# Performance work log

Measured on AMD Instinct MI355X. Metric: run time of the kernel, lower is better.

The kernel has to match this reference:

```python
import jax, jax.numpy as jnp
import numpy as np

B, T, N, DIN, H, E, K, HM, CH, HOR, DOUT = 64, 12, 307, 1, 64, 10, 2, 16, 14, 12, 1
EPS = 1e-12


def setup_inputs() -> dict:
    key = jax.random.key(0)
    ks = jax.random.split(key, 16)
    rn = lambda k, s, sc=0.1: jax.random.normal(k, s, dtype=jnp.float32) * sc
    return {
        "hyper_source": jax.random.normal(ks[0], (B, CH, T, N), dtype=jnp.float32),
        "source": jax.random.normal(ks[1], (B, T, N, DIN), dtype=jnp.float32),
        "adj": jax.random.uniform(ks[2], (N, N), dtype=jnp.float32),
        "node_embeddings": rn(ks[3], (N, E), 1.0),
        "main_weights_pool": rn(ks[4], (E, H, DIN)),
        "hyper_W": rn(ks[5], (CH, H)),
        "hyper_b": jnp.zeros((H,), jnp.float32),
        "mask_W1": rn(ks[6], (H, HM)),
        "mask_W2": rn(ks[7], (HM, E)),
        "gate_Wpool": rn(ks[8], (E, K, 2 * DIN + H, 2 * H)),
        "gate_bpool": rn(ks[9], (E, 2 * H)),
        "upd_Wpool": rn(ks[10], (E, K, 2 * DIN + H, H)),
        "upd_bpool": rn(ks[11], (E, H)),
        "ln_gamma": jnp.ones((H,), jnp.float32),
        "ln_beta": jnp.zeros((H,), jnp.float32),
        "end_W": rn(ks[12], (HOR * DOUT, H)),
        "end_b": jnp.zeros((HOR * DOUT,), jnp.float32),
    }


def _forward(hyper_source, source, adj, node_embeddings, main_weights_pool,
             hyper_W, hyper_b, mask_W1, mask_W2, gate_Wpool, gate_bpool,
             upd_Wpool, upd_bpool, ln_gamma, ln_beta, end_W, end_b):
    # HyperNet: chunked long-history signal -> per-node per-step hidden h [B,N,T,H]
    h = jnp.tanh(jnp.einsum('bctn,ch->bnth', hyper_source, hyper_W) + hyper_b)
    # adaptive input channel: einsum('bnld,ndi->blni') with per-node weights
    weights_h = jnp.einsum('nd,dhi->nhi', node_embeddings, main_weights_pool)  # [N,H,DIN]
    x_adapt = jnp.einsum('bnlh,nhi->blni', h, weights_h)                       # [B,T,N,DIN]
    x = jnp.concatenate([x_adapt, source], axis=-1)                            # [B,T,N,2*DIN]
    # static Chebyshev supports (cheb_k=2): identity + mix(normalized adj, adaptive graph)
    adj_n = adj / jnp.clip(adj.sum(-1, keepdims=True), 1e-6)
    adapt = jax.nn.softmax(jax.nn.relu(node_embeddings @ node_embeddings.T), axis=1)
    A = 0.5 * (adj_n + adapt)
    supports = jnp.stack([jnp.eye(N, dtype=x.dtype), A])                       # [K,N,N]
    # per-node graph-conv weights generated from node embeddings
    gate_W = jnp.einsum('nd,dkio->nkio', node_embeddings, gate_Wpool)
    gate_b = node_embeddings @ gate_bpool
    upd_W = jnp.einsum('nd,dkio->nkio', node_embeddings, upd_Wpool)
    upd_b = node_embeddings @ upd_bpool

    def gconv(sup_b, xin, Wn, bn):
        xg = jnp.einsum('bknm,bmi->bnki', sup_b, xin)
        return jnp.einsum('bnki,nkio->bno', xg, Wn) + bn

    def step(state, inp):
        xt, ht = inp  # [B,N,2*DIN], [B,N,H]
        # dynamic graph sparsification mask from hypernet state
        logits = jnp.einsum('bne,me->bnm', (ht @ mask_W1) @ mask_W2, node_embeddings)
        mask = jax.nn.sigmoid(logits)                # [B,N,N]
        sup_b = supports[None] * mask[:, None]       # [B,K,N,N]
        xs = jnp.concatenate([xt, state], axis=-1)
        zr = jax.nn.sigmoid(gconv(sup_b, xs, gate_W, gate_b))
        z, r = jnp.split(zr, 2, axis=-1)
        cand = jnp.concatenate([xt, z * state], axis=-1)
        hc = jnp.tanh(gconv(sup_b, cand, upd_W, upd_b))
        return r * state + (1.0 - r) * hc, None

    init = jnp.zeros((x.shape[0], N, H), x.dtype)
    state, _ = jax.lax.scan(step, init,
                            (jnp.swapaxes(x, 0, 1), jnp.transpose(h, (2, 0, 1, 3))))
    # layernorm(eps=1e-12); dropout is identity at eval
    mu = state.mean(-1, keepdims=True)
    var = ((state - mu) ** 2).mean(-1, keepdims=True)
    xn = (state - mu) / jnp.sqrt(var + EPS) * ln_gamma + ln_beta
    # end_conv: Conv2d(1, HOR*DOUT, kernel=(1,H)) == per-node linear H -> HOR*DOUT
    out = jnp.einsum('bnh,oh->bon', xn, end_W) + end_b[None, :, None]
    out = out.reshape(-1, HOR, DOUT, N).transpose(0, 1, 3, 2)  # [B,HOR,N,DOUT]
    return out


def reference(hyper_source, source, adj, node_embeddings, main_weights_pool,
              hyper_W, hyper_b, mask_W1, mask_W2, gate_Wpool, gate_bpool,
              upd_Wpool, upd_bpool, ln_gamma, ln_beta, end_W, end_b):
    return _forward(hyper_source, source, adj, node_embeddings, main_weights_pool,
                    hyper_W, hyper_b, mask_W1, mask_W2, gate_Wpool, gate_bpool,
                    upd_Wpool, upd_bpool, ln_gamma, ln_beta, end_W, end_b)
```

## Files before the change

### kernel.cpp

```cpp
#include <hip/hip_runtime.h>
#include <hip/hip_bf16.h>

#define N_ 307
#define B_ 64
#define T_ 12
#define H_ 64
#define E_ 10
#define CH_ 14
#define HM_ 16
#define I2_ 66
#define GO_ 128
#define UO_ 64
#define QG_ (2 * I2_ * GO_)
#define QU_ (2 * I2_ * UO_)

__device__ __forceinline__ float wsum(float v) {
    #pragma unroll
    for (int off = 32; off; off >>= 1) v += __shfl_xor(v, off);
    return v;
}
__device__ __forceinline__ float wmax(float v) {
    #pragma unroll
    for (int off = 32; off; off >>= 1) v = fmaxf(v, __shfl_xor(v, off));
    return v;
}
__device__ __forceinline__ float sigm(float x) { return 1.f / (1.f + __expf(-x)); }
__device__ __forceinline__ float ftanh(float x) { return 1.f - 2.f / (__expf(2.f * x) + 1.f); }

__global__ void A_kernel(const float* __restrict__ adj, const float* __restrict__ nemb,
                         float* __restrict__ A) {
    const int n = blockIdx.x;
    const int lane = threadIdx.x;
    float en[E_];
    #pragma unroll
    for (int d = 0; d < E_; ++d) en[d] = nemb[n * E_ + d];
    float asum = 0.f;
    for (int m = lane; m < N_; m += 64) asum += adj[n * N_ + m];
    asum = fmaxf(wsum(asum), 1e-6f);
    float g[5]; bool valid[5];
    float mx = -1e30f;
    #pragma unroll
    for (int it = 0; it < 5; ++it) {
        int m = lane + it * 64;
        valid[it] = (m < N_);
        float dt = 0.f;
        if (valid[it]) {
            #pragma unroll
            for (int e = 0; e < E_; ++e) dt += en[e] * nemb[m * E_ + e];
            dt = fmaxf(dt, 0.f);
            mx = fmaxf(mx, dt);
        }
        g[it] = dt;
    }
    mx = wmax(mx);
    float se = 0.f;
    #pragma unroll
    for (int it = 0; it < 5; ++it)
        if (valid[it]) { g[it] = __expf(g[it] - mx); se += g[it]; }
    se = wsum(se);
    float inv = 1.f / se;
    #pragma unroll
    for (int it = 0; it < 5; ++it) {
        int m = lane + it * 64;
        if (valid[it]) A[n * N_ + m] = 0.5f * (adj[n * N_ + m] / asum + g[it] * inv);
    }
}

__device__ __forceinline__ float embdot(const float* __restrict__ nemb, int n,
                                        const float* __restrict__ pool, int Q, int q) {
    float a = 0.f;
    #pragma unroll
    for (int d = 0; d < E_; ++d) a += nemb[n * E_ + d] * pool[d * Q + q];
    return a;
}

__global__ __launch_bounds__(256) void gen_kernel(
    const float* __restrict__ nemb,
    const float* __restrict__ gWp, const float* __restrict__ gbp,
    const float* __restrict__ uWp, const float* __restrict__ ubp,
    const float* __restrict__ mwp,
    const float* __restrict__ W1, const float* __restrict__ W2,
    float* __restrict__ gW, float* __restrict__ gb,
    float* __restrict__ uW, float* __restrict__ ub,
    float* __restrict__ wh, float* __restrict__ W12) {
    const int e0 = N_ * QG_;
    const int e1 = e0 + N_ * GO_;
    const int e2 = e1 + N_ * QU_;
    const int e3 = e2 + N_ * UO_;
    const int e4 = e3 + N_ * H_;
    const int e5 = e4 + H_ * E_;
    int idx = blockIdx.x * 256 + threadIdx.x;
    if (idx < e0) {
        int n = idx / QG_, q = idx % QG_;
        gW[idx] = embdot(nemb, n, gWp, QG_, q);
    } else if (idx < e1) {
        int i = idx - e0; int n = i / GO_, q = i % GO_;
        gb[i] = embdot(nemb, n, gbp, GO_, q);
    } else if (idx < e2) {
        int i = idx - e1; int n = i / QU_, q = i % QU_;
        uW[i] = embdot(nemb, n, uWp, QU_, q);
    } else if (idx < e3) {
        int i = idx - e2; int n = i / UO_, q = i % UO_;
        ub[i] = embdot(nemb, n, ubp, UO_, q);
    } else if (idx < e4) {
        int i = idx - e3; int n = i / H_, q = i % H_;
        wh[i] = embdot(nemb, n, mwp, H_, q);
    } else if (idx < e5) {
        int i = idx - e4; int j = i / E_, e = i % E_;
        float a = 0.f;
        #pragma unroll
        for (int q = 0; q < HM_; ++q) a += W1[j * HM_ + q] * W2[q * E_ + e];
        W12[i] = a;
    }
}

__global__ __launch_bounds__(256) void hyper_kernel(
    const float* __restrict__ hs, const float* __restrict__ src,
    const float* __restrict__ hyper_W, const float* __restrict__ hyper_b,
    const float* __restrict__ wh, const float* __restrict__ W12,
    float* __restrict__ x, float* __restrict__ emb) {
    const int wid = blockIdx.x * 4 + (threadIdx.x >> 6);
    const int lane = threadIdx.x & 63;
    const int t = wid / (B_ * N_);
    const int rem = wid % (B_ * N_);
    const int b = rem / N_;
    const int n = rem % N_;
    float acc = hyper_b[lane];
    #pragma unroll
    for (int c = 0; c < CH_; ++c)
        acc += hs[((b * CH_ + c) * T_ + t) * N_ + n] * hyper_W[c * H_ + lane];
    float h = ftanh(acc);
    float x0 = wsum(h * wh[n * H_ + lane]);
    float my_e = 0.f;
    #pragma unroll
    for (int e = 0; e < E_; ++e) {
        float ve = wsum(h * W12[lane * E_ + e]);
        if (lane == e) my_e = ve;
    }
    if (lane < E_) emb[wid * E_ + lane] = my_e;
    if (lane == 0) {
        x[wid * 2] = x0;
        x[wid * 2 + 1] = src[(b * T_ + t) * N_ + n];
    }
}

__global__ __launch_bounds__(256) void maskx_kernel(
    const float* __restrict__ A, const float* __restrict__ emb,
    const float* __restrict__ nemb, const float* __restrict__ x,
    float* __restrict__ dmask, float* __restrict__ aggx) {
    const int wid = blockIdx.x * 4 + (threadIdx.x >> 6);
    const int lane = threadIdx.x & 63;
    const int rem = wid % (B_ * N_);
    const int n = rem % N_;
    float et[E_];
    #pragma unroll
    for (int d = 0; d < E_; ++d) et[d] = emb[wid * E_ + d];
    float a0 = 0.f, a1 = 0.f;
    const int xbase = wid - n;
    for (int m = lane; m < N_; m += 64) {
        float dt = 0.f;
        #pragma unroll
        for (int d = 0; d < E_; ++d) dt += et[d] * nemb[m * E_ + d];
        float sg = sigm(dt);
        if (m == n) dmask[wid] = sg;
        float w = A[n * N_ + m] * sg;
        a0 += w * x[(xbase + m) * 2];
        a1 += w * x[(xbase + m) * 2 + 1];
    }
    a0 = wsum(a0);
    a1 = wsum(a1);
    if (lane == 0) { aggx[wid * 2] = a0; aggx[wid * 2 + 1] = a1; }
}

__global__ __launch_bounds__(256) void aggS_kernel(
    const float* __restrict__ A, const float* __restrict__ emb,
    const float* __restrict__ nemb, const float* __restrict__ Sin,
    float* __restrict__ aggS, int t) {
    __shared__ float emb_s[32][E_];
    __shared__ float ne_s[32][E_];
    __shared__ float w_s[32][33];
    __shared__ float s_s[32][64];
    const int n0 = blockIdx.x * 32;
    const int b = blockIdx.y;
    const int tid = threadIdx.x;
    for (int idx = tid; idx < 32 * E_; idx += 256) {
        int nl = idx / E_, d = idx % E_;
        int n = n0 + nl;
        emb_s[nl][d] = (n < N_) ? emb[((t * B_ + b) * N_ + n) * E_ + d] : 0.f;
    }
    const int ng = tid >> 4, ig = tid & 15;
    const int nl0 = ng * 2, i0 = ig * 4;
    float acc[2][4] = {};
    for (int m0 = 0; m0 < N_; m0 += 32) {
        __syncthreads();
        for (int idx = tid; idx < 32 * E_; idx += 256) {
            int ml = idx / E_, d = idx % E_;
            int m = m0 + ml;
            ne_s[ml][d] = (m < N_) ? nemb[m * E_ + d] : 0.f;
        }
        for (int idx = tid; idx < 32 * 64; idx += 256) {
            int ml = idx >> 6, i = idx & 63;
            int m = m0 + ml;
            s_s[ml][i] = (m < N_) ? Sin[(b * N_ + m) * 64 + i] : 0.f;
        }
        __syncthreads();
        for (int idx = tid; idx < 32 * 32; idx += 256) {
            int nl = idx >> 5, ml = idx & 31;
            int n = n0 + nl, m = m0 + ml;
            float w = 0.f;
            if (n < N_ && m < N_) {
                float dt = 0.f;
                #pragma unroll
                for (int e = 0; e < E_; ++e) dt += emb_s[nl][e] * ne_s[ml][e];
                w = A[n * N_ + m] * sigm(dt);
            }
            w_s[nl][ml] = w;
        }
        __syncthreads();
        #pragma unroll 8
        for (int ml = 0; ml < 32; ++ml) {
            float w0 = w_s[nl0][ml], w1 = w_s[nl0 + 1][ml];
            float4 sv = *(const float4*)&s_s[ml][i0];
            acc[0][0] += w0 * sv.x; acc[0][1] += w0 * sv.y;
            acc[0][2] += w0 * sv.z; acc[0][3] += w0 * sv.w;
            acc[1][0] += w1 * sv.x; acc[1][1] += w1 * sv.y;
            acc[1][2] += w1 * sv.z; acc[1][3] += w1 * sv.w;
        }
    }
    #pragma unroll
    for (int r = 0; r < 2; ++r) {
        int n = n0 + nl0 + r;
        if (n < N_) {
            float4 v = make_float4(acc[r][0], acc[r][1], acc[r][2], acc[r][3]);
            *(float4*)&aggS[(b * N_ + n) * 64 + i0] = v;
        }
    }
}

__global__ __launch_bounds__(256) void gate_mm_kernel(
    const float* __restrict__ gate_W, const float* __restrict__ gate_b,
    const float* __restrict__ x, const float* __restrict__ S,
    const float* __restrict__ dmask, const float* __restrict__ aggx,
    const float* __restrict__ aggS, float* __restrict__ zs,
    float* __restrict__ rbuf, int t) {
    __shared__ float W_s[132][64];
    __shared__ float xg_s[32][132];
    const int oh = blockIdx.x, bh = blockIdx.y, n = blockIdx.z;
    const int tid = threadIdx.x;
    for (int idx = tid; idx < 132 * 64; idx += 256) {
        int row = idx >> 6, op = idx & 63;
        int col = (op < 32) ? (oh * 32 + op) : (64 + oh * 32 + (op - 32));
        W_s[row][op] = gate_W[(n * 132 + row) * GO_ + col];
    }
    for (int idx = tid; idx < 32 * 132; idx += 256) {
        int bl = idx / 132, i = idx % 132;
        int b = bh * 32 + bl;
        int tb = (t * B_ + b) * N_ + n;
        float v;
        if (i < 66) {
            float xs = (i == 0) ? x[tb * 2] : (i == 1) ? x[tb * 2 + 1] : S[(b * N_ + n) * 64 + (i - 2)];
            v = dmask[tb] * xs;
        } else {
            int i2 = i - 66;
            v = (i2 < 2) ? aggx[tb * 2 + i2] : aggS[(b * N_ + n) * 64 + (i2 - 2)];
        }
        xg_s[bl][i] = v;
    }
    __syncthreads();
    const int bl = tid >> 3, og = tid & 7;
    float acc[8] = {};
    for (int i = 0; i < 132; ++i) {
        float xv = xg_s[bl][i];
        #pragma unroll
        for (int r = 0; r < 8; ++r) acc[r] += xv * W_s[i][og * 8 + r];
    }
    float v[8];
    #pragma unroll
    for (int r = 0; r < 8; ++r) {
        int op = og * 8 + r;
        int col = (op < 32) ? (oh * 32 + op) : (64 + oh * 32 + (op - 32));
        v[r] = sigm(acc[r] + gate_b[n * GO_ + col]);
    }
    __syncthreads();
    float* zr_s = &xg_s[0][0];
    #pragma unroll
    for (int r = 0; r < 8; ++r) zr_s[bl * 64 + og * 8 + r] = v[r];
    __syncthreads();
    for (int idx = tid; idx < 32 * 32; idx += 256) {
        int bl2 = idx >> 5, jl = idx & 31;
        int b = bh * 32 + bl2;
        int j = oh * 32 + jl;
        float z = zr_s[bl2 * 64 + jl];
        float rr = zr_s[bl2 * 64 + 32 + jl];
        int sidx = (b * N_ + n) * 64 + j;
        zs[sidx] = z * S[sidx];
        rbuf[sidx] = rr;
    }
}

__global__ __launch_bounds__(256) void upd_mm_kernel(
    const float* __restrict__ upd_W, const float* __restrict__ upd_b,
    const float* __restrict__ x, const float* __restrict__ zsrc,
    const float* __restrict__ dmask, const float* __restrict__ aggx,
    const float* __restrict__ aggS, const float* __restrict__ rbuf,
    float* __restrict__ S, int t) {
    __shared__ float W_s[132][64];
    __shared__ float xg_s[32][132];
    const int bh = blockIdx.x, n = blockIdx.y;
    const int tid = threadIdx.x;
    for (int idx = tid; idx < 132 * 64; idx += 256) {
        int row = idx >> 6, op = idx & 63;
        W_s[row][op] = upd_W[(n * 132 + row) * UO_ + op];
    }
    for (int idx = tid; idx < 32 * 132; idx += 256) {
        int bl = idx / 132, i = idx % 132;
        int b = bh * 32 + bl;
        int tb = (t * B_ + b) * N_ + n;
        float v;
        if (i < 66) {
            float xs = (i == 0) ? x[tb * 2] : (i == 1) ? x[tb * 2 + 1] : zsrc[(b * N_ + n) * 64 + (i - 2)];
            v = dmask[tb] * xs;
        } else {
            int i2 = i - 66;
            v = (i2 < 2) ? aggx[tb * 2 + i2] : aggS[(b * N_ + n) * 64 + (i2 - 2)];
        }
        xg_s[bl][i] = v;
    }
    __syncthreads();
    const int bl = tid >> 3, og = tid & 7;
    float acc[8] = {};
    for (int i = 0; i < 132; ++i) {
        float xv = xg_s[bl][i];
        #pragma unroll
        for (int r = 0; r < 8; ++r) acc[r] += xv * W_s[i][og * 8 + r];
    }
    const int b = bh * 32 + bl;
    #pragma unroll
    for (int r = 0; r < 8; ++r) {
        int op = og * 8 + r;
        float hc = ftanh(acc[r] + upd_b[n * UO_ + op]);
        int sidx = (b * N_ + n) * 64 + op;
        float rr = rbuf[sidx];
        float sv = S[sidx];
        S[sidx] = rr * sv + (1.f - rr) * hc;
    }
}

__global__ __launch_bounds__(256) void final_kernel(
    const float* __restrict__ S, const float* __restrict__ gamma,
    const float* __restrict__ beta, const float* __restrict__ endW,
    const float* __restrict__ endb, float* __restrict__ out) {
    const int wid = blockIdx.x * 4 + (threadIdx.x >> 6);
    const int lane = threadIdx.x & 63;
    const int b = wid / N_, n = wid % N_;
    float s = S[wid * 64 + lane];
    float mu = wsum(s) * (1.f / 64.f);
    float d = s - mu;
    float var = wsum(d * d) * (1.f / 64.f);
    float xn = d / sqrtf(var + 1e-12f) * gamma[lane] + beta[lane];
    #pragma unroll
    for (int o = 0; o < 12; ++o) {
        float dot = wsum(xn * endW[o * 64 + lane]);
        if (lane == o) out[(b * 12 + o) * N_ + n] = dot + endb[o];
    }
}

extern "C" void kernel_launch(void* const* d_in, const int* in_sizes, int n_in,
                              void* d_out, int out_size, void* d_ws, size_t ws_size,
                              hipStream_t stream) {
    const float* hyper_source = (const float*)d_in[0];
    const float* source       = (const float*)d_in[1];
    const float* adj          = (const float*)d_in[2];
    const float* nemb         = (const float*)d_in[3];
    const float* mwpool       = (const float*)d_in[4];
    const float* hyper_W      = (const float*)d_in[5];
    const float* hyper_b      = (const float*)d_in[6];
    const float* mask_W1      = (const float*)d_in[7];
    const float* mask_W2      = (const float*)d_in[8];
    const float* gate_Wpool   = (const float*)d_in[9];
    const float* gate_bpool   = (const float*)d_in[10];
    const float* upd_Wpool    = (const float*)d_in[11];
    const float* upd_bpool    = (const float*)d_in[12];
    const float* ln_gamma     = (const float*)d_in[13];
    const float* ln_beta      = (const float*)d_in[14];
    const float* end_W        = (const float*)d_in[15];
    const float* end_b        = (const float*)d_in[16];
    float* out = (float*)d_out;

    float* ws = (float*)d_ws;
    size_t off = 0;
    auto alloc = [&](size_t nf) {
        float* p = ws + off;
        off += (nf + 255) & ~(size_t)255;
        return p;
    };
    float* A      = alloc((size_t)N_ * N_);
    float* wh     = alloc((size_t)N_ * H_);
    float* W12    = alloc((size_t)H_ * E_);
    float* gate_W = alloc((size_t)N_ * QG_);
    float* gate_b = alloc((size_t)N_ * GO_);
    float* upd_W  = alloc((size_t)N_ * QU_);
    float* upd_b  = alloc((size_t)N_ * UO_);
    float* x      = alloc((size_t)T_ * B_ * N_ * 2);
    float* emb    = alloc((size_t)T_ * B_ * N_ * E_);
    float* dmask  = alloc((size_t)T_ * B_ * N_);
    float* aggx   = alloc((size_t)T_ * B_ * N_ * 2);
    float* S      = alloc((size_t)B_ * N_ * H_);
    float* zs     = alloc((size_t)B_ * N_ * H_);
    float* rbuf   = alloc((size_t)B_ * N_ * H_);
    float* aggS   = alloc((size_t)B_ * N_ * H_);

    hipMemsetAsync(S, 0, (size_t)B_ * N_ * H_ * sizeof(float), stream);

    A_kernel<<<N_, 64, 0, stream>>>(adj, nemb, A);

    const int gen_total = N_ * QG_ + N_ * GO_ + N_ * QU_ + N_ * UO_ + N_ * H_ + H_ * E_;
    gen_kernel<<<(gen_total + 255) / 256, 256, 0, stream>>>(
        nemb, gate_Wpool, gate_bpool, upd_Wpool, upd_bpool, mwpool, mask_W1, mask_W2,
        gate_W, gate_b, upd_W, upd_b, wh, W12);

    const int nwaves = T_ * B_ * N_;
    hyper_kernel<<<nwaves / 4, 256, 0, stream>>>(hyper_source, source, hyper_W, hyper_b, wh,
                                                 W12, x, emb);
    maskx_kernel<<<nwaves / 4, 256, 0, stream>>>(A, emb, nemb, x, dmask, aggx);

    for (int t = 0; t < T_; ++t) {
        aggS_kernel<<<dim3(10, B_), 256, 0, stream>>>(A, emb, nemb, S, aggS, t);
        gate_mm_kernel<<<dim3(2, 2, N_), 256, 0, stream>>>(gate_W, gate_b, x, S, dmask, aggx,
                                                           aggS, zs, rbuf, t);
        aggS_kernel<<<dim3(10, B_), 256, 0, stream>>>(A, emb, nemb, zs, aggS, t);
        upd_mm_kernel<<<dim3(2, N_), 256, 0, stream>>>(upd_W, upd_b, x, zs, dmask, aggx, aggS,
                                                       rbuf, S, t);
    }

    final_kernel<<<(B_ * N_) / 4, 256, 0, stream>>>(S, ln_gamma, ln_beta, end_W, end_b, out);
}
```

Before: 2.720 ms.

## Materialize per-step masked adjacency once and reuse across both graph aggregations

A new per-timestep kernel computes the masked adjacency weights (A times the sigmoid embedding mask) for every batch and node pair into a global buffer. The same kernel also produces dmask and aggx. Both aggS launches in that step then read this precomputed matrix instead of each recomputing the sigmoid dot products. The aggS kernel is rewritten to stage S into LDS in two halves, with each wave producing four output rows. The x buffer is split into two planar arrays. The cost is a 24 MB scratch matrix written and read twice per step, plus an extra launch per timestep.

Measured after the change: 3.037 ms. +11.7%, slower.

```diff
diff --git a/kernel.cpp b/kernel.cpp
--- a/kernel.cpp
+++ b/kernel.cpp
@@ -118,7 +118,7 @@
     const float* __restrict__ hs, const float* __restrict__ src,
     const float* __restrict__ hyper_W, const float* __restrict__ hyper_b,
     const float* __restrict__ wh, const float* __restrict__ W12,
-    float* __restrict__ x, float* __restrict__ emb) {
+    float* __restrict__ x0, float* __restrict__ x1, float* __restrict__ emb) {
     const int wid = blockIdx.x * 4 + (threadIdx.x >> 6);
     const int lane = threadIdx.x & 63;
     const int t = wid / (B_ * N_);
@@ -130,119 +130,114 @@
     for (int c = 0; c < CH_; ++c)
         acc += hs[((b * CH_ + c) * T_ + t) * N_ + n] * hyper_W[c * H_ + lane];
     float h = ftanh(acc);
-    float x0 = wsum(h * wh[n * H_ + lane]);
+    float x0v = wsum(h * wh[n * H_ + lane]);
     float my_e = 0.f;
     #pragma unroll
     for (int e = 0; e < E_; ++e) {
         float ve = wsum(h * W12[lane * E_ + e]);
         if (lane == e) my_e = ve;
     }
-    if (lane < E_) emb[wid * E_ + lane] = my_e;
+    if (lane < E_) emb[(size_t)wid * E_ + lane] = my_e;
     if (lane == 0) {
-        x[wid * 2] = x0;
-        x[wid * 2 + 1] = src[(b * T_ + t) * N_ + n];
-    }
-}
-
-__global__ __launch_bounds__(256) void maskx_kernel(
+        x0[wid] = x0v;
+        x1[wid] = src[(b * T_ + t) * N_ + n];
+    }
+}
+
+__global__ __launch_bounds__(256) void wm_kernel(
     const float* __restrict__ A, const float* __restrict__ emb,
-    const float* __restrict__ nemb, const float* __restrict__ x,
-    float* __restrict__ dmask, float* __restrict__ aggx) {
-    const int wid = blockIdx.x * 4 + (threadIdx.x >> 6);
+    const float* __restrict__ nemb, const float* __restrict__ x0,
+    const float* __restrict__ x1, float* __restrict__ Wm,
+    float* __restrict__ dmask, float* __restrict__ aggx, int t) {
+    const int wid = __builtin_amdgcn_readfirstlane(blockIdx.x * 4 + (threadIdx.x >> 6));
     const int lane = threadIdx.x & 63;
-    const int rem = wid % (B_ * N_);
-    const int n = rem % N_;
+    const int b = wid / N_;
+    const int n = wid % N_;
+    const int tbn = (t * B_ + b) * N_ + n;
+    const int xb = tbn - n;
     float et[E_];
     #pragma unroll
-    for (int d = 0; d < E_; ++d) et[d] = emb[wid * E_ + d];
+    for (int d = 0; d < E_; ++d) et[d] = emb[(size_t)tbn * E_ + d];
+    float* wr = Wm + (size_t)(b * N_ + n) * N_;
     float a0 = 0.f, a1 = 0.f;
-    const int xbase = wid - n;
-    for (int m = lane; m < N_; m += 64) {
+    #pragma unroll
+    for (int c = 0; c < 5; ++c) {
+        int m = c * 64 + lane;
+        bool v = (m < N_);
+        int mc = v ? m : 0;
         float dt = 0.f;
         #pragma unroll
-        for (int d = 0; d < E_; ++d) dt += et[d] * nemb[m * E_ + d];
+        for (int d = 0; d < E_; ++d) dt += et[d] * nemb[mc * E_ + d];
         float sg = sigm(dt);
-        if (m == n) dmask[wid] = sg;
-        float w = A[n * N_ + m] * sg;
-        a0 += w * x[(xbase + m) * 2];
-        a1 += w * x[(xbase + m) * 2 + 1];
+        float w = v ? A[n * N_ + mc] * sg : 0.f;
+        if (v) {
+            wr[m] = w;
+            if (m == n) dmask[tbn] = sg;
+            a0 += w * x0[xb + mc];
+            a1 += w * x1[xb + mc];
+        }
     }
     a0 = wsum(a0);
     a1 = wsum(a1);
-    if (lane == 0) { aggx[wid * 2] = a0; aggx[wid * 2 + 1] = a1; }
-}
-
-__global__ __launch_bounds__(256) void aggS_kernel(
-    const float* __restrict__ A, const float* __restrict__ emb,
-    const float* __restrict__ nemb, const float* __restrict__ Sin,
-    float* __restrict__ aggS, int t) {
-    __shared__ float emb_s[32][E_];
-    __shared__ float ne_s[32][E_];
-    __shared__ float w_s[32][33];
-    __shared__ float s_s[32][64];
-    const int n0 = blockIdx.x * 32;
+    if (lane == 0) {
+        aggx[(size_t)tbn * 2] = a0;
+        aggx[(size_t)tbn * 2 + 1] = a1;
+    }
+}
+
+__global__ __launch_bounds__(512) void aggS_kernel(
+    const float* __restrict__ Wm, const float* __restrict__ Sin,
+    float* __restrict__ aggS) {
+    __shared__ float s_lds[160 * 64];
+    const int tid = threadIdx.x;
+    const int lane = tid & 63;
+    const int wv = __builtin_amdgcn_readfirstlane(tid >> 6);
     const int b = blockIdx.y;
-    const int tid = threadIdx.x;
-    for (int idx = tid; idx < 32 * E_; idx += 256) {
-        int nl = idx / E_, d = idx % E_;
-        int n = n0 + nl;
-        emb_s[nl][d] = (n < N_) ? emb[((t * B_ + b) * N_ + n) * E_ + d] : 0.f;
-    }
-    const int ng = tid >> 4, ig = tid & 15;
-    const int nl0 = ng * 2, i0 = ig * 4;
-    float acc[2][4] = {};
-    for (int m0 = 0; m0 < N_; m0 += 32) {
-        __syncthreads();
-        for (int idx = tid; idx < 32 * E_; idx += 256) {
-            int ml = idx / E_, d = idx % E_;
-            int m = m0 + ml;
-            ne_s[ml][d] = (m < N_) ? nemb[m * E_ + d] : 0.f;
-        }
-        for (int idx = tid; idx < 32 * 64; idx += 256) {
-            int ml = idx >> 6, i = idx & 63;
-            int m = m0 + ml;
-            s_s[ml][i] = (m < N_) ? Sin[(b * N_ + m) * 64 + i] : 0.f;
-        }
-        __syncthreads();
-        for (int idx = tid; idx < 32 * 32; idx += 256) {
-            int nl = idx >> 5, ml = idx & 31;
-            int n = n0 + nl, m = m0 + ml;
-            float w = 0.f;
-            if (n < N_ && m < N_) {
-                float dt = 0.f;
-                #pragma unroll
-                for (int e = 0; e < E_; ++e) dt += emb_s[nl][e] * ne_s[ml][e];
-                w = A[n * N_ + m] * sigm(dt);
-            }
-            w_s[nl][ml] = w;
-        }
-        __syncthreads();
-        #pragma unroll 8
-        for (int ml = 0; ml < 32; ++ml) {
-            float w0 = w_s[nl0][ml], w1 = w_s[nl0 + 1][ml];
-            float4 sv = *(const float4*)&s_s[ml][i0];
-            acc[0][0] += w0 * sv.x; acc[0][1] += w0 * sv.y;
-            acc[0][2] += w0 * sv.z; acc[0][3] += w0 * sv.w;
-            acc[1][0] += w1 * sv.x; acc[1][1] += w1 * sv.y;
-            acc[1][2] += w1 * sv.z; acc[1][3] += w1 * sv.w;
-        }
-    }
-    #pragma unroll
-    for (int r = 0; r < 2; ++r) {
-        int n = n0 + nl0 + r;
-        if (n < N_) {
-            float4 v = make_float4(acc[r][0], acc[r][1], acc[r][2], acc[r][3]);
-            *(float4*)&aggS[(b * N_ + n) * 64 + i0] = v;
-        }
+    const int nb = blockIdx.x * 32 + wv * 4;
+    int roff[4];
+    #pragma unroll
+    for (int r = 0; r < 4; ++r) {
+        int nr = nb + r; if (nr > N_ - 1) nr = N_ - 1;
+        roff[r] = __builtin_amdgcn_readfirstlane((b * N_ + nr) * N_);
+    }
+    float acc[4] = {0.f, 0.f, 0.f, 0.f};
+    float4* d4 = (float4*)s_lds;
+    {
+        const float4* s4 = (const float4*)(Sin + (size_t)b * N_ * H_);
+        for (int idx = tid; idx < 160 * 16; idx += 512) d4[idx] = s4[idx];
+    }
+    __syncthreads();
+    #pragma unroll 8
+    for (int m = 0; m < 160; ++m) {
+        float sv = s_lds[m * 64 + lane];
+        #pragma unroll
+        for (int r = 0; r < 4; ++r) acc[r] = fmaf(Wm[roff[r] + m], sv, acc[r]);
+    }
+    __syncthreads();
+    {
+        const float4* s4 = (const float4*)(Sin + ((size_t)b * N_ + 160) * H_);
+        for (int idx = tid; idx < 147 * 16; idx += 512) d4[idx] = s4[idx];
+    }
+    __syncthreads();
+    #pragma unroll 8
+    for (int m = 0; m < 147; ++m) {
+        float sv = s_lds[m * 64 + lane];
+        #pragma unroll
+        for (int r = 0; r < 4; ++r) acc[r] = fmaf(Wm[roff[r] + 160 + m], sv, acc[r]);
+    }
+    #pragma unroll
+    for (int r = 0; r < 4; ++r) {
+        int nr = nb + r;
+        if (nr < N_) aggS[((size_t)b * N_ + nr) * H_ + lane] = acc[r];
     }
 }
 
 __global__ __launch_bounds__(256) void gate_mm_kernel(
     const float* __restrict__ gate_W, const float* __restrict__ gate_b,
-    const float* __restrict__ x, const float* __restrict__ S,
-    const float* __restrict__ dmask, const float* __restrict__ aggx,
-    const float* __restrict__ aggS, float* __restrict__ zs,
-    float* __restrict__ rbuf, int t) {
+    const float* __restrict__ x0, const float* __restrict__ x1,
+    const float* __restrict__ S, const float* __restrict__ dmask,
+    const float* __restrict__ aggx, const float* __restrict__ aggS,
+    float* __restrict__ zs, float* __restrict__ rbuf, int t) {
     __shared__ float W_s[132][64];
     __shared__ float xg_s[32][132];
     const int oh = blockIdx.x, bh = blockIdx.y, n = blockIdx.z;
@@ -258,11 +253,11 @@
         int tb = (t * B_ + b) * N_ + n;
         float v;
         if (i < 66) {
-            float xs = (i == 0) ? x[tb * 2] : (i == 1) ? x[tb * 2 + 1] : S[(b * N_ + n) * 64 + (i - 2)];
+            float xs = (i == 0) ? x0[tb] : (i == 1) ? x1[tb] : S[(b * N_ + n) * 64 + (i - 2)];
             v = dmask[tb] * xs;
         } else {
             int i2 = i - 66;
-            v = (i2 < 2) ? aggx[tb * 2 + i2] : aggS[(b * N_ + n) * 64 + (i2 - 2)];
+            v = (i2 < 2) ? aggx[(size_t)tb * 2 + i2] : aggS[(b * N_ + n) * 64 + (i2 - 2)];
         }
         xg_s[bl][i] = v;
     }
@@ -300,10 +295,10 @@
 
 __global__ __launch_bounds__(256) void upd_mm_kernel(
     const float* __restrict__ upd_W, const float* __restrict__ upd_b,
-    const float* __restrict__ x, const float* __restrict__ zsrc,
-    const float* __restrict__ dmask, const float* __restrict__ aggx,
-    const float* __restrict__ aggS, const float* __restrict__ rbuf,
-    float* __restrict__ S, int t) {
+    const float* __restrict__ x0, const float* __restrict__ x1,
+    const float* __restrict__ zsrc, const float* __restrict__ dmask,
+    const float* __restrict__ aggx, const float* __restrict__ aggS,
+    const float* __restrict__ rbuf, float* __restrict__ S, int t) {
     __shared__ float W_s[132][64];
     __shared__ float xg_s[32][132];
     const int bh = blockIdx.x, n = blockIdx.y;
@@ -318,11 +313,11 @@
         int tb = (t * B_ + b) * N_ + n;
         float v;
         if (i < 66) {
-            float xs = (i == 0) ? x[tb * 2] : (i == 1) ? x[tb * 2 + 1] : zsrc[(b * N_ + n) * 64 + (i - 2)];
+            float xs = (i == 0) ? x0[tb] : (i == 1) ? x1[tb] : zsrc[(b * N_ + n) * 64 + (i - 2)];
             v = dmask[tb] * xs;
         } else {
             int i2 = i - 66;
-            v = (i2 < 2) ? aggx[tb * 2 + i2] : aggS[(b * N_ + n) * 64 + (i2 - 2)];
+            v = (i2 < 2) ? aggx[(size_t)tb * 2 + i2] : aggS[(b * N_ + n) * 64 + (i2 - 2)];
         }
         xg_s[bl][i] = v;
     }
@@ -401,7 +396,8 @@
     float* gate_b = alloc((size_t)N_ * GO_);
     float* upd_W  = alloc((size_t)N_ * QU_);
     float* upd_b  = alloc((size_t)N_ * UO_);
-    float* x      = alloc((size_t)T_ * B_ * N_ * 2);
+    float* x0     = alloc((size_t)T_ * B_ * N_);
+    float* x1     = alloc((size_t)T_ * B_ * N_);
     float* emb    = alloc((size_t)T_ * B_ * N_ * E_);
     float* dmask  = alloc((size_t)T_ * B_ * N_);
     float* aggx   = alloc((size_t)T_ * B_ * N_ * 2);
@@ -409,6 +405,7 @@
     float* zs     = alloc((size_t)B_ * N_ * H_);
     float* rbuf   = alloc((size_t)B_ * N_ * H_);
     float* aggS   = alloc((size_t)B_ * N_ * H_);
+    float* Wm     = alloc((size_t)B_ * N_ * N_);
 
     hipMemsetAsync(S, 0, (size_t)B_ * N_ * H_ * sizeof(float), stream);
 
@@ -421,16 +418,16 @@
 
     const int nwaves = T_ * B_ * N_;
     hyper_kernel<<<nwaves / 4, 256, 0, stream>>>(hyper_source, source, hyper_W, hyper_b, wh,
-                                                 W12, x, emb);
-    maskx_kernel<<<nwaves / 4, 256, 0, stream>>>(A, emb, nemb, x, dmask, aggx);
+                                                 W12, x0, x1, emb);
 
     for (int t = 0; t < T_; ++t) {
-        aggS_kernel<<<dim3(10, B_), 256, 0, stream>>>(A, emb, nemb, S, aggS, t);
-        gate_mm_kernel<<<dim3(2, 2, N_), 256, 0, stream>>>(gate_W, gate_b, x, S, dmask, aggx,
-                                                           aggS, zs, rbuf, t);
-        aggS_kernel<<<dim3(10, B_), 256, 0, stream>>>(A, emb, nemb, zs, aggS, t);
-        upd_mm_kernel<<<dim3(2, N_), 256, 0, stream>>>(upd_W, upd_b, x, zs, dmask, aggx, aggS,
-                                                       rbuf, S, t);
+        wm_kernel<<<(B_ * N_) / 4, 256, 0, stream>>>(A, emb, nemb, x0, x1, Wm, dmask, aggx, t);
+        aggS_kernel<<<dim3(10, B_), 512, 0, stream>>>(Wm, S, aggS);
+        gate_mm_kernel<<<dim3(2, 2, N_), 256, 0, stream>>>(gate_W, gate_b, x0, x1, S, dmask,
+                                                           aggx, aggS, zs, rbuf, t);
+        aggS_kernel<<<dim3(10, B_), 512, 0, stream>>>(Wm, zs, aggS);
+        upd_mm_kernel<<<dim3(2, N_), 256, 0, stream>>>(upd_W, upd_b, x0, x1, zs, dmask, aggx,
+                                                       aggS, rbuf, S, t);
     }
 
     final_kernel<<<(B_ * N_) / 4, 256, 0, stream>>>(S, ln_gamma, ln_beta, end_W, end_b, out);
```
